# Optimization experiments

Hardware: AMD Instinct MI355X
Metric: run time of the kernel (lower is better)

## Reference

```python
import jax, jax.numpy as jnp
import numpy as np

P = 256          # patches per (batch*time) element
EPS = 1e-6
WEIGHT_SIM = 1.0
WEIGHT_GRAM = 10.0


def setup_inputs() -> dict:
    key = jax.random.key(0)
    k1, k2 = jax.random.split(key)
    N, D = 16384, 768  # N = bt * P with bt = 64
    inp = jax.random.normal(k1, (N, D), dtype=jnp.float32)
    tgt = jax.random.normal(k2, (N, D), dtype=jnp.float32)
    return {"input": inp, "target": tgt}


def _l2n(x):
    return x / jnp.sqrt(jnp.sum(x * x, axis=-1, keepdims=True)).clip(1e-12)


def reference(input, target):
    target = jax.lax.stop_gradient(target)
    N, D = input.shape
    bt = N // P

    input_n = _l2n(input)
    target_n = _l2n(target)

    input_view = input.reshape(bt, P, D)
    target_view = target.reshape(bt, P, D)
    in_n = input_n.reshape(bt, P, D)
    tg_n = target_n.reshape(bt, P, D)

    # gram of normalized targets; its row-mean gives tf
    gram_gt = jnp.einsum('bpd,bqd->bpq', tg_n, tg_n)           # [bt, P, P]
    tf = 1.0 / (gram_gt.mean(axis=-1) + EPS)                    # [bt, P]

    # cross_sim.mean(dim=-1) == all_patches @ mean(all_patches): O(N*d) not O(N^2*d)
    mean_patch = target_n.mean(axis=0)                          # [D]
    cross_mean = target_n @ mean_patch                          # [N]
    idf = 1.0 / (cross_mean.reshape(bt, P) + EPS)               # [bt, P]

    weights = tf * idf
    weights = weights / (weights.sum(axis=1, keepdims=True) + EPS)

    patch_loss = jnp.mean((input_view - target_view) ** 2, axis=-1)  # [bt, P]
    sim_loss = jnp.mean(jnp.sum(weights * patch_loss, axis=1))

    gram_pred = jnp.einsum('bpd,bqd->bpq', in_n, in_n)          # [bt, P, P]
    diff2 = (gram_pred - gram_gt) ** 2
    pair_w = weights[:, :, None] * weights[:, None, :]          # [bt, P, P]
    gram_loss = jnp.mean(jnp.sum(pair_w * diff2, axis=(1, 2)))

    return WEIGHT_SIM * sim_loss + WEIGHT_GRAM * gram_loss
```

## Files before the change

kernel.cpp:

```cpp
#include <hip/hip_runtime.h>
#include <hip/hip_bf16.h>

#define NROWS 16384
#define DIM   768
#define PP    256
#define BT    64
#define EPSF  1e-6f
#define GKC   32
#define NTILE 10
#define NGRAM (BT * NTILE)

typedef short          bf16x8 __attribute__((ext_vector_type(8)));
typedef float          f32x4  __attribute__((ext_vector_type(4)));
typedef unsigned short us8    __attribute__((ext_vector_type(8)));

__device__ __forceinline__ unsigned short f2bf(float x) {
    __hip_bfloat16 h = __float2bfloat16(x);
    return *reinterpret_cast<unsigned short*>(&h);
}

template<int PRE>
__global__ __launch_bounds__(512) void k_norms(const float* __restrict__ in,
                                               const float* __restrict__ tg,
                                               float* __restrict__ inv_in,
                                               float* __restrict__ inv_tg,
                                               float* __restrict__ ploss,
                                               unsigned short* __restrict__ in_n,
                                               unsigned short* __restrict__ tg_n) {
    const int row = blockIdx.x * 16 + (threadIdx.x >> 5);
    const int c   = threadIdx.x & 31;
    const float4* ip = (const float4*)(in + (size_t)row * DIM);
    const float4* tp = (const float4*)(tg + (size_t)row * DIM);
    float4 a[6], t[6];
#pragma unroll
    for (int k = 0; k < 3; ++k) {
        a[2*k]   = ip[2*c + 64*k];     a[2*k+1] = ip[2*c + 64*k + 1];
        t[2*k]   = tp[2*c + 64*k];     t[2*k+1] = tp[2*c + 64*k + 1];
    }
    float si = 0.f, st = 0.f, sd = 0.f;
#pragma unroll
    for (int k = 0; k < 6; ++k) {
        si += a[k].x*a[k].x + a[k].y*a[k].y + a[k].z*a[k].z + a[k].w*a[k].w;
        st += t[k].x*t[k].x + t[k].y*t[k].y + t[k].z*t[k].z + t[k].w*t[k].w;
        float dx = a[k].x-t[k].x, dy = a[k].y-t[k].y, dz = a[k].z-t[k].z, dw = a[k].w-t[k].w;
        sd += dx*dx + dy*dy + dz*dz + dw*dw;
    }
#pragma unroll
    for (int o = 16; o; o >>= 1) {
        si += __shfl_xor(si, o); st += __shfl_xor(st, o); sd += __shfl_xor(sd, o);
    }
    float ii = 1.f / fmaxf(sqrtf(si), 1e-12f);
    float it = 1.f / fmaxf(sqrtf(st), 1e-12f);
    if (c == 0) { inv_in[row] = ii; inv_tg[row] = it; ploss[row] = sd * (1.f / DIM); }
    if constexpr (PRE != 0) {
#pragma unroll
        for (int k = 0; k < 3; ++k) {
            us8 ua, ut;
            ua[0]=f2bf(a[2*k].x*ii);  ua[1]=f2bf(a[2*k].y*ii);
            ua[2]=f2bf(a[2*k].z*ii);  ua[3]=f2bf(a[2*k].w*ii);
            ua[4]=f2bf(a[2*k+1].x*ii);ua[5]=f2bf(a[2*k+1].y*ii);
            ua[6]=f2bf(a[2*k+1].z*ii);ua[7]=f2bf(a[2*k+1].w*ii);
            ut[0]=f2bf(t[2*k].x*it);  ut[1]=f2bf(t[2*k].y*it);
            ut[2]=f2bf(t[2*k].z*it);  ut[3]=f2bf(t[2*k].w*it);
            ut[4]=f2bf(t[2*k+1].x*it);ut[5]=f2bf(t[2*k+1].y*it);
            ut[6]=f2bf(t[2*k+1].z*it);ut[7]=f2bf(t[2*k+1].w*it);
            *(us8*)(in_n + (size_t)row * DIM + 8*c + 256*k) = ua;
            *(us8*)(tg_n + (size_t)row * DIM + 8*c + 256*k) = ut;
        }
    }
}


__global__ __launch_bounds__(64) void k_bsum1(const float* __restrict__ tg,
                                              const float* __restrict__ inv_tg,
                                              float* __restrict__ psum) {
    int b = blockIdx.x, y = blockIdx.y, h = blockIdx.z;
    int d0 = y * 256 + threadIdx.x * 4;
    const float* base = tg + (size_t)(b * PP + h * 64) * DIM + d0;
    const float* itg  = inv_tg + b * PP + h * 64;
    float4 s = { 0.f, 0.f, 0.f, 0.f };
    for (int r = 0; r < 64; ++r) {
        float4 v = *(const float4*)(base + (size_t)r * DIM);
        float w = itg[r];
        s.x += v.x * w; s.y += v.y * w; s.z += v.z * w; s.w += v.w * w;
    }
    *(float4*)(psum + (size_t)(b * 4 + h) * DIM + d0) = s;
}

__global__ __launch_bounds__(256) void k_bsum2(const float* __restrict__ psum,
                                               float* __restrict__ bsum,
                                               float* __restrict__ va) {
    int d = blockIdx.x * 256 + threadIdx.x;
    if (d >= DIM) return;
    float g = 0.f;
    for (int b = 0; b < BT; ++b) {
        float s = psum[(size_t)(b * 4 + 0) * DIM + d] + psum[(size_t)(b * 4 + 1) * DIM + d]
                + psum[(size_t)(b * 4 + 2) * DIM + d] + psum[(size_t)(b * 4 + 3) * DIM + d];
        bsum[b * DIM + d] = s;
        g += s;
    }
    va[d] = g * (1.f / NROWS);
}

__global__ __launch_bounds__(256) void k_wdots(const float* __restrict__ tg,
                                               const float* __restrict__ inv_tg,
                                               const float* __restrict__ bsum,
                                               const float* __restrict__ va,
                                               float* __restrict__ wraw) {
    int wave = threadIdx.x >> 6, lane = threadIdx.x & 63;
    int gw = blockIdx.x * 4 + wave;
#pragma unroll
    for (int rr = 0; rr < 4; ++rr) {
        int row = gw * 4 + rr;
        int b   = row >> 8;
        const float4* t4 = (const float4*)(tg + (size_t)row * DIM);
        const float4* b4 = (const float4*)(bsum + b * DIM);
        const float4* a4 = (const float4*)va;
        float db = 0.f, da = 0.f;
#pragma unroll
        for (int v = 0; v < 3; ++v) {
            float4 t = t4[lane + 64 * v];
            float4 x = b4[lane + 64 * v];
            float4 y = a4[lane + 64 * v];
            db += t.x * x.x + t.y * x.y + t.z * x.z + t.w * x.w;
            da += t.x * y.x + t.y * y.y + t.z * y.z + t.w * y.w;
        }
#pragma unroll
        for (int o = 32; o; o >>= 1) { db += __shfl_xor(db, o); da += __shfl_xor(da, o); }
        if (lane == 0) {
            float itg = inv_tg[row];
            db *= itg; da *= itg;
            wraw[row] = (1.f / (db * (1.f / PP) + EPSF)) * (1.f / (da + EPSF));
        }
    }
}

__global__ __launch_bounds__(256) void k_wfinal(const float* __restrict__ wraw,
                                                const float* __restrict__ ploss,
                                                float* __restrict__ weights,
                                                float* __restrict__ simpart) {
    __shared__ float red[256];
    int b = blockIdx.x, p = threadIdx.x, row = b * PP + p;
    float w = wraw[row];
    red[p] = w; __syncthreads();
    for (int s = 128; s; s >>= 1) { if (p < s) red[p] += red[p + s]; __syncthreads(); }
    float wn = w / (red[0] + EPSF);
    weights[row] = wn;
    __syncthreads();
    red[p] = wn * ploss[row]; __syncthreads();
    for (int s = 128; s; s >>= 1) { if (p < s) red[p] += red[p + s]; __syncthreads(); }
    if (p == 0) simpart[b] = red[0];
}

__global__ __launch_bounds__(256, 3) void k_gram(const unsigned short* __restrict__ in_n,
                                                 const unsigned short* __restrict__ tg_n,
                                                 const float* __restrict__ weights,
                                                 float* __restrict__ grampart) {
    __shared__ __align__(16) unsigned short L[2][4][64 * GKC];
    __shared__ float red[256];

    const int wg  = blockIdx.x;
    const int xcd = wg & 7, j = wg >> 3;
    const int b   = xcd * 8 + j / NTILE;
    const int t   = j % NTILE;
    int ti, tj;
    if (t < 4)      { ti = 0; tj = t; }
    else if (t < 7) { ti = 1; tj = t - 3; }
    else if (t < 9) { ti = 2; tj = t - 5; }
    else            { ti = 3; tj = 3; }
    const int pr = ti * 64, qc = tj * 64;
    const bool diag = (ti == tj);
    const float factor = diag ? 1.f : 2.f;
    const int bP = b * PP;

    const int tid = threadIdx.x, lane = tid & 63, wave = tid >> 6;

    const unsigned short* smat = (wave & 1) ? tg_n : in_n;
    const int  srow0   = bP + ((wave < 2) ? pr : qc);
    const bool doStage = !(diag && wave >= 2);
    const int  srl = lane >> 2;
    const int  scc = lane & 3;
    const int  wcc = scc ^ (srl & 3);

    us8 sreg[4];
    auto LD = [&](int k0) {
        if (!doStage) return;
#pragma unroll
        for (int i = 0; i < 4; ++i)
            sreg[i] = *(const us8*)(smat + (size_t)(srow0 + 16 * i + srl) * DIM + k0 + scc * 8);
    };
    auto WR = [&](int cur) {
        if (!doStage) return;
#pragma unroll
        for (int i = 0; i < 4; ++i)
            *(us8*)&L[cur][wave][(16 * i + srl) * GKC + wcc * 8] = sreg[i];
    };

    const int ar0 = (wave >> 1) * 32, bc0 = (wave & 1) * 32;
    const int rl = lane & 15, kc = lane >> 4;
    const int bi_ = diag ? 0 : 2, bt_ = diag ? 1 : 3;

    f32x4 accI[2][2], accT[2][2];
#pragma unroll
    for (int m = 0; m < 2; ++m)
#pragma unroll
        for (int n = 0; n < 2; ++n) {
            f32x4 z = { 0.f, 0.f, 0.f, 0.f };
            accI[m][n] = z; accT[m][n] = z;
        }

    LD(0); WR(0);
    int cur = 0;
    const int NS = DIM / GKC;
    for (int ks = 0; ks < NS; ++ks) {
        if (ks + 1 < NS) LD((ks + 1) * GKC);
        __syncthreads();
        bf16x8 aI[2], aT[2], bI[2], bT[2];
#pragma unroll
        for (int m = 0; m < 2; ++m) {
            int row = ar0 + m * 16 + rl;
            int off = row * GKC + ((kc ^ (row & 3)) << 3);
            aI[m] = *(const bf16x8*)&L[cur][0][off];
            aT[m] = *(const bf16x8*)&L[cur][1][off];
        }
#pragma unroll
        for (int n = 0; n < 2; ++n) {
            int row = bc0 + n * 16 + rl;
            int off = row * GKC + ((kc ^ (row & 3)) << 3);
            bI[n] = *(const bf16x8*)&L[cur][bi_][off];
            bT[n] = *(const bf16x8*)&L[cur][bt_][off];
        }
#pragma unroll
        for (int m = 0; m < 2; ++m)
#pragma unroll
            for (int n = 0; n < 2; ++n) {
                accI[m][n] = __builtin_amdgcn_mfma_f32_16x16x32_bf16(aI[m], bI[n], accI[m][n], 0, 0, 0);
                accT[m][n] = __builtin_amdgcn_mfma_f32_16x16x32_bf16(aT[m], bT[n], accT[m][n], 0, 0, 0);
            }
        if (ks + 1 < NS) WR(cur ^ 1);
        cur ^= 1;
    }

    const int r4 = lane >> 4, cl = lane & 15;
    float wq[2], wp[2][4];
#pragma unroll
    for (int n = 0; n < 2; ++n) wq[n] = weights[bP + qc + bc0 + n * 16 + cl];
#pragma unroll
    for (int m = 0; m < 2; ++m)
#pragma unroll
        for (int r = 0; r < 4; ++r) wp[m][r] = weights[bP + pr + ar0 + m * 16 + r4 * 4 + r];
    float local = 0.f;
#pragma unroll
    for (int m = 0; m < 2; ++m)
#pragma unroll
        for (int n = 0; n < 2; ++n)
#pragma unroll
            for (int r = 0; r < 4; ++r) {
                float d = accI[m][n][r] - accT[m][n][r];
                local += wp[m][r] * wq[n] * d * d;
            }
    local *= factor;
    red[tid] = local; __syncthreads();
    for (int s = 128; s; s >>= 1) { if (tid < s) red[tid] += red[tid + s]; __syncthreads(); }
    if (tid == 0) grampart[wg] = red[0];
}

#define LP 40
__global__ __launch_bounds__(256) void k_gram_f32(const float* __restrict__ in,
                                                  const float* __restrict__ tg,
                                                  const float* __restrict__ inv_in,
                                                  const float* __restrict__ inv_tg,
                                                  const float* __restrict__ weights,
                                                  float* __restrict__ grampart) {
    __shared__ __align__(16) unsigned short LA0[128 * LP];
    __shared__ __align__(16) unsigned short LA1[128 * LP];
    __shared__ __align__(16) unsigned short LB0[128 * LP];
    __shared__ __align__(16) unsigned short LB1[128 * LP];
    __shared__ float red[256];

    const int wg  = blockIdx.x;
    const int xcd = wg & 7, j = wg >> 3;
    const int b   = xcd * 8 + j / 3;
    const int t3  = j % 3;
    const int pr  = (t3 == 2) ? 128 : 0;
    const int qc  = (t3 == 0) ? 0 : 128;
    const bool diag = (pr == qc);
    const float factor = diag ? 1.f : 2.f;

    const int tid  = threadIdx.x;
    const int lane = tid & 63;
    const int wave = tid >> 6;
    const int wr = (wave >> 1) * 64, wc = (wave & 1) * 64;
    const int bP = b * PP;

    const int strow = tid >> 2;
    const int skq   = tid & 3;
    const int sw    = (strow >> 3) & 3;

    const float* srcf[4] = { in, tg, in, tg };
    unsigned short* ldst[4] = { LA0, LA1, LB0, LB1 };

    size_t g[4][2];
#pragma unroll
    for (int h = 0; h < 2; ++h) {
        g[0][h] = (size_t)(bP + pr + strow + h * 64) * DIM + skq * 8;
        g[1][h] = g[0][h];
        g[2][h] = (size_t)(bP + qc + strow + h * 64) * DIM + skq * 8;
        g[3][h] = g[2][h];
    }
    float scl[4][2];
#pragma unroll
    for (int h = 0; h < 2; ++h) {
        scl[0][h] = inv_in[bP + pr + strow + h * 64];
        scl[1][h] = inv_tg[bP + pr + strow + h * 64];
        scl[2][h] = inv_in[bP + qc + strow + h * 64];
        scl[3][h] = inv_tg[bP + qc + strow + h * 64];
    }

    float4 pfa[4][2], pfb[4][2];

    auto STAGE_LOAD = [&](int k0) {
#pragma unroll
        for (int bi = 0; bi < 4; ++bi) {
            if (bi >= 2 && diag) continue;
#pragma unroll
            for (int h = 0; h < 2; ++h) {
                pfa[bi][h] = *(const float4*)(srcf[bi] + g[bi][h] + k0);
                pfb[bi][h] = *(const float4*)(srcf[bi] + g[bi][h] + k0 + 4);
            }
        }
    };
    auto STAGE_WRITE = [&]() {
#pragma unroll
        for (int bi = 0; bi < 4; ++bi) {
            if (bi >= 2 && diag) continue;
#pragma unroll
            for (int h = 0; h < 2; ++h) {
                us8 v;
                float s = scl[bi][h];
                float4 x = pfa[bi][h], y = pfb[bi][h];
                v[0] = f2bf(x.x * s); v[1] = f2bf(x.y * s);
                v[2] = f2bf(x.z * s); v[3] = f2bf(x.w * s);
                v[4] = f2bf(y.x * s); v[5] = f2bf(y.y * s);
                v[6] = f2bf(y.z * s); v[7] = f2bf(y.w * s);
                int row = strow + h * 64;
                *(us8*)&ldst[bi][row * LP + (skq ^ sw) * 8] = v;
            }
        }
    };

    const unsigned short* RB0 = diag ? LA0 : LB0;
    const unsigned short* RB1 = diag ? LA1 : LB1;

    f32x4 accI[4][4], accT[4][4];
#pragma unroll
    for (int m = 0; m < 4; ++m)
#pragma unroll
        for (int n = 0; n < 4; ++n) {
            f32x4 z = { 0.f, 0.f, 0.f, 0.f };
            accI[m][n] = z; accT[m][n] = z;
        }

    STAGE_LOAD(0);
    for (int ks = 0; ks < DIM / GKC; ++ks) {
        __syncthreads();
        STAGE_WRITE();
        __syncthreads();
        if (ks + 1 < DIM / GKC) STAGE_LOAD(GKC * (ks + 1));

        bf16x8 aI[4], aT[4], bI[4], bT[4];
#pragma unroll
        for (int m = 0; m < 4; ++m) {
            int row = wr + m * 16 + (lane & 15);
            int off = row * LP + (((lane >> 4) ^ ((row >> 3) & 3))) * 8;
            aI[m] = *(const bf16x8*)&LA0[off];
            aT[m] = *(const bf16x8*)&LA1[off];
        }
#pragma unroll
        for (int n = 0; n < 4; ++n) {
            int row = wc + n * 16 + (lane & 15);
            int off = row * LP + (((lane >> 4) ^ ((row >> 3) & 3))) * 8;
            bI[n] = *(const bf16x8*)&RB0[off];
            bT[n] = *(const bf16x8*)&RB1[off];
        }
#pragma unroll
        for (int m = 0; m < 4; ++m)
#pragma unroll
            for (int n = 0; n < 4; ++n) {
                accI[m][n] = __builtin_amdgcn_mfma_f32_16x16x32_bf16(aI[m], bI[n], accI[m][n], 0, 0, 0);
                accT[m][n] = __builtin_amdgcn_mfma_f32_16x16x32_bf16(aT[m], bT[n], accT[m][n], 0, 0, 0);
            }
    }

    const int r4 = lane >> 4, cl = lane & 15;
    float wq[4], wp[4][4];
#pragma unroll
    for (int n = 0; n < 4; ++n) wq[n] = weights[bP + qc + wc + n * 16 + cl];
#pragma unroll
    for (int m = 0; m < 4; ++m)
#pragma unroll
        for (int r = 0; r < 4; ++r) wp[m][r] = weights[bP + pr + wr + m * 16 + r4 * 4 + r];
    float local = 0.f;
#pragma unroll
    for (int m = 0; m < 4; ++m)
#pragma unroll
        for (int n = 0; n < 4; ++n)
#pragma unroll
            for (int r = 0; r < 4; ++r) {
                float d = accI[m][n][r] - accT[m][n][r];
                local += wp[m][r] * wq[n] * d * d;
            }
    local *= factor;
    red[tid] = local; __syncthreads();
    for (int s = 128; s; s >>= 1) { if (tid < s) red[tid] += red[tid + s]; __syncthreads(); }
    if (tid == 0) grampart[wg] = red[0];
}

__global__ __launch_bounds__(256) void k_final(const float* __restrict__ simpart,
                                               const float* __restrict__ grampart,
                                               int ngram,
                                               float* __restrict__ out) {
    __shared__ float red[256];
    int t = threadIdx.x;
    float v = (t < BT) ? simpart[t] : 0.f;
    float g = 0.f;
    for (int i = t; i < ngram; i += 256) g += grampart[i];
    v += 10.f * g;
    red[t] = v; __syncthreads();
    for (int s = 128; s; s >>= 1) { if (t < s) red[t] += red[t + s]; __syncthreads(); }
    if (t == 0) out[0] = red[0] * (1.f / BT);
}

extern "C" void kernel_launch(void* const* d_in, const int* in_sizes, int n_in,
                              void* d_out, int out_size, void* d_ws, size_t ws_size,
                              hipStream_t stream) {
    (void)in_sizes; (void)n_in; (void)out_size;
    const float* in = (const float*)d_in[0];
    const float* tg = (const float*)d_in[1];

    const size_t bfBytes   = (size_t)NROWS * DIM * 2;
    const size_t floatsOff = 2 * bfBytes;
    const size_t fCount    = 5 * (size_t)NROWS + 5 * (size_t)BT * DIM + DIM + BT + NGRAM;
    const size_t needed    = floatsOff + fCount * 4;
    const bool   pre       = ws_size >= needed;

    char* wsb = (char*)d_ws;
    unsigned short* in_n = nullptr;
    unsigned short* tg_n = nullptr;
    float* fbase;
    if (pre) {
        in_n  = (unsigned short*)wsb;
        tg_n  = (unsigned short*)(wsb + bfBytes);
        fbase = (float*)(wsb + floatsOff);
    } else {
        fbase = (float*)wsb;
    }
    float* inv_in  = fbase;
    float* inv_tg  = fbase + NROWS;
    float* ploss   = fbase + 2 * (size_t)NROWS;
    float* wraw    = fbase + 3 * (size_t)NROWS;
    float* weights = fbase + 4 * (size_t)NROWS;
    float* psum    = fbase + 5 * (size_t)NROWS;
    float* bsum    = psum + 4 * (size_t)BT * DIM;
    float* va      = bsum + (size_t)BT * DIM;
    float* simpart = va + DIM;
    float* grampart= simpart + BT;

    if (pre) {
        k_norms<1><<<NROWS / 16, 512, 0, stream>>>(in, tg, inv_in, inv_tg, ploss, in_n, tg_n);
    } else {
        k_norms<0><<<NROWS / 16, 512, 0, stream>>>(in, tg, inv_in, inv_tg, ploss, nullptr, nullptr);
    }
    k_bsum1<<<dim3(BT, 3, 4), 64, 0, stream>>>(tg, inv_tg, psum);
    k_bsum2<<<3, 256, 0, stream>>>(psum, bsum, va);
    k_wdots<<<NROWS / 16, 256, 0, stream>>>(tg, inv_tg, bsum, va, wraw);
    k_wfinal<<<BT, 256, 0, stream>>>(wraw, ploss, weights, simpart);
    if (pre) {
        k_gram<<<NGRAM, 256, 0, stream>>>(in_n, tg_n, weights, grampart);
        k_final<<<1, 256, 0, stream>>>(simpart, grampart, NGRAM, (float*)d_out);
    } else {
        k_gram_f32<<<192, 256, 0, stream>>>(in, tg, inv_in, inv_tg, weights, grampart);
        k_final<<<1, 256, 0, stream>>>(simpart, grampart, 192, (float*)d_out);
    }
}
```

Before: 79.14 us.

## Fuse per-batch normalized target column sums into the norms kernel

The norms kernel now writes each row's normalized target into shared memory and reduces 8 rows per workgroup into a partial column sum. This removes the separate k_bsum1 pass, which re-read the whole target matrix from global memory. The per-batch sum and the global mean are split into two small kernels. The trade-off is a new shared buffer and a barrier in the norms kernel, smaller workgroups, and a much larger psum buffer (2048×768 floats) that the next kernel must read.

```diff
diff --git a/kernel.cpp b/kernel.cpp
--- a/kernel.cpp
+++ b/kernel.cpp
@@ -9,6 +9,8 @@
 #define GKC   32
 #define NTILE 10
 #define NGRAM (BT * NTILE)
+#define SPITCH 776
+#define NWG_N  (NROWS / 8)
 
 typedef short          bf16x8 __attribute__((ext_vector_type(8)));
 typedef float          f32x4  __attribute__((ext_vector_type(4)));
@@ -20,22 +22,25 @@
 }
 
 template<int PRE>
-__global__ __launch_bounds__(512) void k_norms(const float* __restrict__ in,
+__global__ __launch_bounds__(256) void k_norms(const float* __restrict__ in,
                                                const float* __restrict__ tg,
                                                float* __restrict__ inv_in,
                                                float* __restrict__ inv_tg,
                                                float* __restrict__ ploss,
                                                unsigned short* __restrict__ in_n,
-                                               unsigned short* __restrict__ tg_n) {
-    const int row = blockIdx.x * 16 + (threadIdx.x >> 5);
+                                               unsigned short* __restrict__ tg_n,
+                                               float* __restrict__ psum) {
+    __shared__ __align__(16) float S[8][SPITCH];
+    const int r   = threadIdx.x >> 5;
     const int c   = threadIdx.x & 31;
+    const int row = blockIdx.x * 8 + r;
     const float4* ip = (const float4*)(in + (size_t)row * DIM);
     const float4* tp = (const float4*)(tg + (size_t)row * DIM);
     float4 a[6], t[6];
 #pragma unroll
     for (int k = 0; k < 3; ++k) {
-        a[2*k]   = ip[2*c + 64*k];     a[2*k+1] = ip[2*c + 64*k + 1];
-        t[2*k]   = tp[2*c + 64*k];     t[2*k+1] = tp[2*c + 64*k + 1];
+        a[2*k]   = ip[2*c + 64*k];  a[2*k+1] = ip[2*c + 64*k + 1];
+        t[2*k]   = tp[2*c + 64*k];  t[2*k+1] = tp[2*c + 64*k + 1];
     }
     float si = 0.f, st = 0.f, sd = 0.f;
 #pragma unroll
@@ -52,6 +57,16 @@
     float ii = 1.f / fmaxf(sqrtf(si), 1e-12f);
     float it = 1.f / fmaxf(sqrtf(st), 1e-12f);
     if (c == 0) { inv_in[row] = ii; inv_tg[row] = it; ploss[row] = sd * (1.f / DIM); }
+
+#pragma unroll
+    for (int k = 0; k < 3; ++k) {
+        float4 u0 = t[2*k], u1 = t[2*k+1];
+        u0.x*=it; u0.y*=it; u0.z*=it; u0.w*=it;
+        u1.x*=it; u1.y*=it; u1.z*=it; u1.w*=it;
+        *(float4*)&S[r][8*c + 256*k]     = u0;
+        *(float4*)&S[r][8*c + 256*k + 4] = u1;
+    }
+
     if constexpr (PRE != 0) {
 #pragma unroll
         for (int k = 0; k < 3; ++k) {
@@ -68,37 +83,34 @@
             *(us8*)(tg_n + (size_t)row * DIM + 8*c + 256*k) = ut;
         }
     }
-}
-
-
-__global__ __launch_bounds__(64) void k_bsum1(const float* __restrict__ tg,
-                                              const float* __restrict__ inv_tg,
-                                              float* __restrict__ psum) {
-    int b = blockIdx.x, y = blockIdx.y, h = blockIdx.z;
-    int d0 = y * 256 + threadIdx.x * 4;
-    const float* base = tg + (size_t)(b * PP + h * 64) * DIM + d0;
-    const float* itg  = inv_tg + b * PP + h * 64;
-    float4 s = { 0.f, 0.f, 0.f, 0.f };
-    for (int r = 0; r < 64; ++r) {
-        float4 v = *(const float4*)(base + (size_t)r * DIM);
-        float w = itg[r];
-        s.x += v.x * w; s.y += v.y * w; s.z += v.z * w; s.w += v.w * w;
-    }
-    *(float4*)(psum + (size_t)(b * 4 + h) * DIM + d0) = s;
-}
+
+    __syncthreads();
+#pragma unroll
+    for (int q = 0; q < 3; ++q) {
+        int d = threadIdx.x + 256 * q;
+        float s = 0.f;
+#pragma unroll
+        for (int rr = 0; rr < 8; ++rr) s += S[rr][d];
+        psum[(size_t)blockIdx.x * DIM + d] = s;
+    }
+}
+
 
 __global__ __launch_bounds__(256) void k_bsum2(const float* __restrict__ psum,
-                                               float* __restrict__ bsum,
+                                               float* __restrict__ bsum) {
+    int b = blockIdx.x, d = blockIdx.y * 256 + threadIdx.x;
+    float s = 0.f;
+#pragma unroll 8
+    for (int i = 0; i < 32; ++i)
+        s += psum[(size_t)(b * 32 + i) * DIM + d];
+    bsum[b * DIM + d] = s;
+}
+
+__global__ __launch_bounds__(256) void k_gmean(const float* __restrict__ bsum,
                                                float* __restrict__ va) {
     int d = blockIdx.x * 256 + threadIdx.x;
-    if (d >= DIM) return;
     float g = 0.f;
-    for (int b = 0; b < BT; ++b) {
-        float s = psum[(size_t)(b * 4 + 0) * DIM + d] + psum[(size_t)(b * 4 + 1) * DIM + d]
-                + psum[(size_t)(b * 4 + 2) * DIM + d] + psum[(size_t)(b * 4 + 3) * DIM + d];
-        bsum[b * DIM + d] = s;
-        g += s;
-    }
+    for (int b = 0; b < BT; ++b) g += bsum[b * DIM + d];
     va[d] = g * (1.f / NROWS);
 }
 
@@ -440,7 +452,8 @@
 
     const size_t bfBytes   = (size_t)NROWS * DIM * 2;
     const size_t floatsOff = 2 * bfBytes;
-    const size_t fCount    = 5 * (size_t)NROWS + 5 * (size_t)BT * DIM + DIM + BT + NGRAM;
+    const size_t fCount    = 5 * (size_t)NROWS + (size_t)NWG_N * DIM
+                           + (size_t)BT * DIM + DIM + BT + NGRAM;
     const size_t needed    = floatsOff + fCount * 4;
     const bool   pre       = ws_size >= needed;
 
@@ -461,18 +474,18 @@
     float* wraw    = fbase + 3 * (size_t)NROWS;
     float* weights = fbase + 4 * (size_t)NROWS;
     float* psum    = fbase + 5 * (size_t)NROWS;
-    float* bsum    = psum + 4 * (size_t)BT * DIM;
+    float* bsum    = psum + (size_t)NWG_N * DIM;
     float* va      = bsum + (size_t)BT * DIM;
     float* simpart = va + DIM;
     float* grampart= simpart + BT;
 
     if (pre) {
-        k_norms<1><<<NROWS / 16, 512, 0, stream>>>(in, tg, inv_in, inv_tg, ploss, in_n, tg_n);
+        k_norms<1><<<NWG_N, 256, 0, stream>>>(in, tg, inv_in, inv_tg, ploss, in_n, tg_n, psum);
     } else {
-        k_norms<0><<<NROWS / 16, 512, 0, stream>>>(in, tg, inv_in, inv_tg, ploss, nullptr, nullptr);
-    }
-    k_bsum1<<<dim3(BT, 3, 4), 64, 0, stream>>>(tg, inv_tg, psum);
-    k_bsum2<<<3, 256, 0, stream>>>(psum, bsum, va);
+        k_norms<0><<<NWG_N, 256, 0, stream>>>(in, tg, inv_in, inv_tg, ploss, nullptr, nullptr, psum);
+    }
+    k_bsum2<<<dim3(BT, 3), 256, 0, stream>>>(psum, bsum);
+    k_gmean<<<3, 256, 0, stream>>>(bsum, va);
     k_wdots<<<NROWS / 16, 256, 0, stream>>>(tg, inv_tg, bsum, va, wraw);
     k_wfinal<<<BT, 256, 0, stream>>>(wraw, ploss, weights, simpart);
     if (pre) {
```

Measured after the change: 69.61 us. 1.14x faster.
